# Performance work log

Hardware: AMD Instinct MI355X
Metric: run time of the kernel (lower is better)

## Reference

```python
import jax, jax.numpy as jnp
import numpy as np

CHAN = 128
IN_CHAN = 64
N_LAY = 4
N_OUT = 1000


def _affine_sample(img, theta):
    """F.affine_grid + F.grid_sample (bilinear, zeros padding, align_corners=False).
    img: [B, C, H, W]; theta: [C, 2, 3] (one affine per channel, shared over batch).
    """
    B, C, H, W = img.shape
    dt = img.dtype
    xs = (jnp.arange(W, dtype=dt) + 0.5) * (2.0 / W) - 1.0
    ys = (jnp.arange(H, dtype=dt) + 0.5) * (2.0 / H) - 1.0
    gx, gy = jnp.meshgrid(xs, ys)                      # [H, W] (xy indexing)
    base = jnp.stack([gx, gy, jnp.ones_like(gx)], -1)  # [H, W, 3]
    grid = jnp.einsum('cij,hwj->chwi', theta, base)    # [C, H, W, 2] (x, y)
    ix = ((grid[..., 0] + 1.0) * W - 1.0) * 0.5        # unnormalize, align_corners=False
    iy = ((grid[..., 1] + 1.0) * H - 1.0) * 0.5
    x0 = jnp.floor(ix)
    y0 = jnp.floor(iy)
    wx1 = ix - x0
    wy1 = iy - y0
    x0i = x0.astype(jnp.int32)
    y0i = y0.astype(jnp.int32)
    cidx = jnp.arange(C)[:, None, None]

    def tap(yi, xi, w):
        valid = (xi >= 0) & (xi < W) & (yi >= 0) & (yi < H)
        v = img[:, cidx, jnp.clip(yi, 0, H - 1), jnp.clip(xi, 0, W - 1)]  # [B,C,H,W]
        return v * (w * valid.astype(dt))[None]

    return (tap(y0i, x0i, (1 - wy1) * (1 - wx1))
            + tap(y0i, x0i + 1, (1 - wy1) * wx1)
            + tap(y0i + 1, x0i, wy1 * (1 - wx1))
            + tap(y0i + 1, x0i + 1, wy1 * wx1))


def _geom_layer(x, lin, geo, box):
    # expand-multiply-sum channel mix == einsum
    mixed = jnp.einsum('ci,bihw->bchw', lin, x)        # [B, chan, H, W]
    b = _affine_sample(jnp.ones_like(mixed), box)      # warped box of ones
    w = _affine_sample(mixed, geo)                     # warped features
    return w * b


def setup_inputs() -> dict:
    key = jax.random.key(0)
    ks = jax.random.split(key, 10)
    eye = jnp.eye(3, dtype=jnp.float32)[:2]            # [2, 3]
    x = jax.random.normal(ks[0], (16, IN_CHAN, 96, 96), dtype=jnp.float32)
    in_geo = eye[None] + 0.1 * jax.random.normal(ks[1], (CHAN, 2, 3), dtype=jnp.float32)
    in_box = eye[None] + 0.1 * jax.random.normal(ks[2], (CHAN, 2, 3), dtype=jnp.float32)
    in_lin = jax.random.uniform(ks[3], (CHAN, IN_CHAN), dtype=jnp.float32)
    lay_geo = eye[None, None] + 0.1 * jax.random.normal(ks[4], (N_LAY, CHAN, 2, 3), dtype=jnp.float32)
    lay_box = eye[None, None] + 0.1 * jax.random.normal(ks[5], (N_LAY, CHAN, 2, 3), dtype=jnp.float32)
    lay_lin = jax.random.uniform(ks[6], (N_LAY, CHAN, CHAN), dtype=jnp.float32)
    bound = 1.0 / np.sqrt(CHAN)
    dense_w = jax.random.uniform(ks[7], (N_OUT, CHAN), dtype=jnp.float32, minval=-bound, maxval=bound)
    dense_b = jax.random.uniform(ks[8], (N_OUT,), dtype=jnp.float32, minval=-bound, maxval=bound)
    return {"x": x, "in_geo": in_geo, "in_box": in_box, "in_lin": in_lin,
            "lay_geo": lay_geo, "lay_box": lay_box, "lay_lin": lay_lin,
            "dense_w": dense_w, "dense_b": dense_b}


def reference(x, in_geo, in_box, in_lin, lay_geo, lay_box, lay_lin, dense_w, dense_b):
    x = _geom_layer(x, in_lin, in_geo, in_box)
    for i in range(lay_lin.shape[0]):                  # resCon=True
        x = _geom_layer(x, lay_lin[i], lay_geo[i], lay_box[i]) + x
    feat_maps = x
    pooled = feat_maps.mean(axis=(-2, -1))             # [B, chan]
    logits = pooled @ dense_w.T + dense_b              # [B, nbOut]
    return (logits, feat_maps)
```

## Files before the change

kernel.cpp:

```cpp
#include <hip/hip_runtime.h>
#include <stdint.h>

#define HW 96
#define NPIX 9216
#define NCH 128
#define NB 16
#define HP 98

using bf16x8 = __attribute__((ext_vector_type(8))) short;
using f32x4  = __attribute__((ext_vector_type(4))) float;

__device__ inline uint32_t packbf(float v) {
    uint32_t u  = __float_as_uint(v);
    uint32_t rh = (u + 0x7FFFu + ((u >> 16) & 1u)) & 0xFFFF0000u;
    float    lo = v - __uint_as_float(rh);
    uint32_t ul = __float_as_uint(lo);
    uint32_t rl = ((ul + 0x7FFFu + ((ul >> 16) & 1u)) >> 16) & 0xFFFFu;
    return rh | rl;
}

__global__ __launch_bounds__(256) void packlin_kernel(const float* __restrict__ lin,
                                                      uint32_t* __restrict__ linP, int n) {
    const int i = blockIdx.x * 256 + threadIdx.x;
    if (i < n) linP[i] = packbf(lin[i]);
}

template<int K>
__global__ __launch_bounds__(512, 4) void mix_kernel(const float* __restrict__ x,
                                                     const float* __restrict__ lin,
                                                     float* __restrict__ mixed) {
    const int b    = blockIdx.y;
    const int lane = threadIdx.x & 63;
    const int p    = blockIdx.x * 128 + lane * 2;
    const int c0   = __builtin_amdgcn_readfirstlane((threadIdx.x >> 6) * 16);
    const float* xb = x + (size_t)b * K * NPIX + p;
    const float* lr = lin + c0 * K;

    float2 acc[16];
    #pragma unroll
    for (int c = 0; c < 16; ++c) acc[c] = float2{0.f, 0.f};

    for (int k0 = 0; k0 < K; k0 += 8) {
        float2 xv[8];
        #pragma unroll
        for (int j = 0; j < 8; ++j)
            xv[j] = *(const float2*)&xb[(size_t)(k0 + j) * NPIX];
        #pragma unroll
        for (int c = 0; c < 16; ++c) {
            const float* lc = lr + c * K + k0;
            #pragma unroll
            for (int j = 0; j < 8; ++j) {
                acc[c].x = fmaf(lc[j], xv[j].x, acc[c].x);
                acc[c].y = fmaf(lc[j], xv[j].y, acc[c].y);
            }
        }
    }
    float* ob = mixed + (size_t)b * NCH * NPIX + p;
    #pragma unroll
    for (int c = 0; c < 16; ++c)
        *(float2*)&ob[(size_t)(c0 + c) * NPIX] = acc[c];
}

template<int K>
__global__ __launch_bounds__(512, 2) void mix_mfma_kernel(const float* __restrict__ xf,
                                                          const uint32_t* __restrict__ lp,
                                                          float* __restrict__ mixed) {
    __shared__ uint32_t xs[K * 128];
    const int b   = blockIdx.y;
    const int px0 = blockIdx.x * 128;
    const int t   = threadIdx.x;

    const float* xb = xf + (size_t)b * K * NPIX + px0;
    #pragma unroll
    for (int i = 0; i < K / 16; ++i) {
        const int f4  = i * 512 + t;
        const int row = f4 >> 5;
        const int c4  = (f4 & 31) << 2;
        const float4 v = *(const float4*)&xb[(size_t)row * NPIX + c4];
        uint4 pv;
        pv.x = packbf(v.x); pv.y = packbf(v.y); pv.z = packbf(v.z); pv.w = packbf(v.w);
        *(uint4*)&xs[row * 128 + (c4 ^ ((row & 0xC) << 2))] = pv;
    }

    const int l  = t & 63;
    const int wv = t >> 6;
    const int c0 = wv * 16;
    const int lq = l >> 4;
    const int lr = l & 15;

    constexpr int NQ = K / 32;
    bf16x8 AH[NQ], AL[NQ];
    const uint32_t* lrow = lp + (size_t)(c0 + lr) * K;
    #pragma unroll
    for (int q = 0; q < NQ; ++q) {
        const uint4 a0 = *(const uint4*)&lrow[q * 32 + lq * 4];
        const uint4 a1 = *(const uint4*)&lrow[q * 32 + 16 + lq * 4];
        union { uint32_t w[4]; bf16x8 v; } h, m;
        h.w[0] = (a0.x >> 16) | (a0.y & 0xFFFF0000u);
        h.w[1] = (a0.z >> 16) | (a0.w & 0xFFFF0000u);
        h.w[2] = (a1.x >> 16) | (a1.y & 0xFFFF0000u);
        h.w[3] = (a1.z >> 16) | (a1.w & 0xFFFF0000u);
        m.w[0] = (a0.x & 0xFFFFu) | (a0.y << 16);
        m.w[1] = (a0.z & 0xFFFFu) | (a0.w << 16);
        m.w[2] = (a1.x & 0xFFFFu) | (a1.y << 16);
        m.w[3] = (a1.z & 0xFFFFu) | (a1.w << 16);
        AH[q] = h.v; AL[q] = m.v;
    }

    f32x4 acc[8];
    #pragma unroll
    for (int n = 0; n < 8; ++n) acc[n] = f32x4{0.f, 0.f, 0.f, 0.f};

    __syncthreads();

    const int pswz = lq << 4;
    #pragma unroll
    for (int q = 0; q < NQ; ++q) {
        const int kb = q * 32 + lq * 4;
        #pragma unroll
        for (int np = 0; np < 4; ++np) {
            const int n0 = np * 2;
            bf16x8 BH0, BL0, BH1, BL1;
            #pragma unroll
            for (int s = 0; s < 2; ++s) {
                const int px = ((n0 + s) * 16 + lr) ^ pswz;
                const uint32_t u0 = xs[(kb + 0) * 128 + px];
                const uint32_t u1 = xs[(kb + 1) * 128 + px];
                const uint32_t u2 = xs[(kb + 2) * 128 + px];
                const uint32_t u3 = xs[(kb + 3) * 128 + px];
                const uint32_t u4 = xs[(kb + 16) * 128 + px];
                const uint32_t u5 = xs[(kb + 17) * 128 + px];
                const uint32_t u6 = xs[(kb + 18) * 128 + px];
                const uint32_t u7 = xs[(kb + 19) * 128 + px];
                union { uint32_t w[4]; bf16x8 v; } h, m;
                h.w[0] = (u0 >> 16) | (u1 & 0xFFFF0000u);
                h.w[1] = (u2 >> 16) | (u3 & 0xFFFF0000u);
                h.w[2] = (u4 >> 16) | (u5 & 0xFFFF0000u);
                h.w[3] = (u6 >> 16) | (u7 & 0xFFFF0000u);
                m.w[0] = (u0 & 0xFFFFu) | (u1 << 16);
                m.w[1] = (u2 & 0xFFFFu) | (u3 << 16);
                m.w[2] = (u4 & 0xFFFFu) | (u5 << 16);
                m.w[3] = (u6 & 0xFFFFu) | (u7 << 16);
                if (s == 0) { BH0 = h.v; BL0 = m.v; } else { BH1 = h.v; BL1 = m.v; }
            }
            acc[n0]     = __builtin_amdgcn_mfma_f32_16x16x32_bf16(AH[q], BH0, acc[n0],     0, 0, 0);
            acc[n0 + 1] = __builtin_amdgcn_mfma_f32_16x16x32_bf16(AH[q], BH1, acc[n0 + 1], 0, 0, 0);
            acc[n0]     = __builtin_amdgcn_mfma_f32_16x16x32_bf16(AH[q], BL0, acc[n0],     0, 0, 0);
            acc[n0 + 1] = __builtin_amdgcn_mfma_f32_16x16x32_bf16(AH[q], BL1, acc[n0 + 1], 0, 0, 0);
            acc[n0]     = __builtin_amdgcn_mfma_f32_16x16x32_bf16(AL[q], BH0, acc[n0],     0, 0, 0);
            acc[n0 + 1] = __builtin_amdgcn_mfma_f32_16x16x32_bf16(AL[q], BH1, acc[n0 + 1], 0, 0, 0);
            acc[n0]     = __builtin_amdgcn_mfma_f32_16x16x32_bf16(AL[q], BL0, acc[n0],     0, 0, 0);
            acc[n0 + 1] = __builtin_amdgcn_mfma_f32_16x16x32_bf16(AL[q], BL1, acc[n0 + 1], 0, 0, 0);
        }
    }

    float* ob = mixed + ((size_t)b * NCH + c0 + lq * 4) * NPIX + px0 + lr;
    #pragma unroll
    for (int n = 0; n < 8; ++n)
        #pragma unroll
        for (int r = 0; r < 4; ++r)
            ob[(size_t)r * NPIX + n * 16] = acc[n][r];
}

__device__ inline float clamp01(float z) { return fminf(fmaxf(z, 0.f), 1.f); }

template<bool RES, bool POOL>
__global__ __launch_bounds__(512) void sample_kernel(const float* __restrict__ mixed,
                                                     const float* __restrict__ geo,
                                                     const float* __restrict__ box,
                                                     float* __restrict__ out,
                                                     float* __restrict__ pooled) {
    __shared__ float m[HP * HP];
    const int c = blockIdx.x;
    const int b = blockIdx.y;
    const int t = threadIdx.x;
    if (t < HP) {
        m[t] = 0.f;
        m[(HP - 1) * HP + t] = 0.f;
    } else if (t < HP + 96) {
        const int h = t - HP + 1;
        m[h * HP] = 0.f;
        m[h * HP + HP - 1] = 0.f;
    }
    const float* src = mixed + ((size_t)b * NCH + c) * NPIX;
    #pragma unroll
    for (int r = 0; r < NPIX / 512; ++r) {
        const int idx = r * 512 + t;
        const int h = idx / 96, w = idx - (idx / 96) * 96;
        m[(h + 1) * HP + (w + 1)] = src[idx];
    }
    const float* gth = geo + c * 6;
    const float* bth = box + c * 6;
    const float g0 = gth[0], g1 = gth[1], g3 = gth[3], g4 = gth[4];
    const float gcx = 48.f * gth[2] - 47.5f * (g0 + g1) + 47.5f;
    const float gcy = 48.f * gth[5] - 47.5f * (g3 + g4) + 47.5f;
    const float b0 = bth[0], b1 = bth[1], b3 = bth[3], b4 = bth[4];
    const float bcx = 48.f * bth[2] - 47.5f * (b0 + b1) + 47.5f;
    const float bcy = 48.f * bth[5] - 47.5f * (b3 + b4) + 47.5f;
    float* o = out + ((size_t)b * NCH + c) * NPIX;
    __syncthreads();
    float psum = 0.f;
    #pragma unroll 6
    for (int r = 0; r < NPIX / 512; ++r) {
        const int p = r * 512 + t;
        const int h = p / 96, w = p - (p / 96) * 96;
        const float fw = (float)w, fh = (float)h;
        float ix = fmaf(g0, fw, fmaf(g1, fh, gcx));
        float iy = fmaf(g3, fw, fmaf(g4, fh, gcy));
        ix = fminf(fmaxf(ix, -1.f), 96.f);
        iy = fminf(fmaxf(iy, -1.f), 96.f);
        const float x0f = floorf(ix), y0f = floorf(iy);
        const float fx = ix - x0f, fy = iy - y0f;
        const int base = ((int)y0f + 1) * HP + ((int)x0f + 1);
        const float m00 = m[base],      m01 = m[base + 1];
        const float m10 = m[base + HP], m11 = m[base + HP + 1];
        const float mx0 = fmaf(fx, m01 - m00, m00);
        const float mx1 = fmaf(fx, m11 - m10, m10);
        float v = fmaf(fy, mx1 - mx0, mx0);
        const float bx = fmaf(b0, fw, fmaf(b1, fh, bcx));
        const float by = fmaf(b3, fw, fmaf(b4, fh, bcy));
        const float Xs = fminf(clamp01(bx + 1.f), clamp01(96.f - bx));
        const float Ys = fminf(clamp01(by + 1.f), clamp01(96.f - by));
        v *= Xs * Ys;
        if (RES) v += o[p];
        o[p] = v;
        if (POOL) psum += v;
    }
    if (POOL) {
        #pragma unroll
        for (int off = 32; off > 0; off >>= 1) psum += __shfl_down(psum, off, 64);
        __shared__ float red[8];
        if ((t & 63) == 0) red[t >> 6] = psum;
        __syncthreads();
        if (t == 0) {
            float s = 0.f;
            #pragma unroll
            for (int i = 0; i < 8; ++i) s += red[i];
            pooled[b * NCH + c] = s * (1.f / (float)NPIX);
        }
    }
}

__global__ __launch_bounds__(256) void pool_kernel(const float* __restrict__ feat,
                                                   float* __restrict__ pooled) {
    const int bc = blockIdx.x;
    const float4* f = (const float4*)(feat + (size_t)bc * NPIX);
    float s = 0.f;
    for (int i = threadIdx.x; i < NPIX / 4; i += 256) {
        const float4 v = f[i];
        s += (v.x + v.y) + (v.z + v.w);
    }
    #pragma unroll
    for (int off = 32; off > 0; off >>= 1) s += __shfl_down(s, off, 64);
    __shared__ float red[4];
    if ((threadIdx.x & 63) == 0) red[threadIdx.x >> 6] = s;
    __syncthreads();
    if (threadIdx.x == 0)
        pooled[bc] = (red[0] + red[1] + red[2] + red[3]) * (1.f / (float)NPIX);
}

__global__ __launch_bounds__(256) void dense_kernel(const float* __restrict__ pooled,
                                                    const float* __restrict__ Wt,
                                                    const float* __restrict__ bias,
                                                    float* __restrict__ out) {
    const int idx = blockIdx.x * 256 + threadIdx.x;
    if (idx >= NB * 1000) return;
    const int b = idx / 1000, n = idx - b * 1000;
    float acc = bias[n];
    const float* p = pooled + b * NCH;
    const float* wr = Wt + n * NCH;
    #pragma unroll 4
    for (int c = 0; c < NCH; ++c) acc = fmaf(p[c], wr[c], acc);
    out[idx] = acc;
}

extern "C" void kernel_launch(void* const* d_in, const int* in_sizes, int n_in,
                              void* d_out, int out_size, void* d_ws, size_t ws_size,
                              hipStream_t stream) {
    const float* x       = (const float*)d_in[0];
    const float* in_geo  = (const float*)d_in[1];
    const float* in_box  = (const float*)d_in[2];
    const float* in_lin  = (const float*)d_in[3];
    const float* lay_geo = (const float*)d_in[4];
    const float* lay_box = (const float*)d_in[5];
    const float* lay_lin = (const float*)d_in[6];
    const float* dense_w = (const float*)d_in[7];
    const float* dense_b = (const float*)d_in[8];

    float* out  = (float*)d_out;
    float* feat = out + NB * 1000;
    float* mixed = (float*)d_ws;

    const size_t mixedFloats = (size_t)NB * NCH * NPIX;
    const size_t linPWords   = 4 * NCH * NCH + NCH * 64;
    const bool fusedPool = ws_size >= (mixedFloats + NB * NCH) * sizeof(float);
    const bool mfmaOK    = ws_size >= (mixedFloats + NB * NCH + linPWords) * sizeof(float);
    float* pooled = fusedPool ? (float*)d_ws + mixedFloats : (float*)d_ws;

    const dim3 mixGrid(NPIX / 128, NB);
    const dim3 smpGrid(NCH, NB);

    if (mfmaOK) {
        uint32_t* linP  = (uint32_t*)((float*)d_ws + mixedFloats + NB * NCH);
        uint32_t* linP0 = linP + 4 * NCH * NCH;
        packlin_kernel<<<(4 * NCH * NCH + 255) / 256, 256, 0, stream>>>(lay_lin, linP, 4 * NCH * NCH);
        packlin_kernel<<<(NCH * 64 + 255) / 256, 256, 0, stream>>>(in_lin, linP0, NCH * 64);
        mix_mfma_kernel<64><<<mixGrid, 512, 0, stream>>>(x, linP0, mixed);
        sample_kernel<false, false><<<smpGrid, 512, 0, stream>>>(mixed, in_geo, in_box, feat, pooled);
        for (int i = 0; i < 3; ++i) {
            mix_mfma_kernel<128><<<mixGrid, 512, 0, stream>>>(feat, linP + (size_t)i * NCH * NCH, mixed);
            sample_kernel<true, false><<<smpGrid, 512, 0, stream>>>(mixed, lay_geo + i * NCH * 6,
                                                                    lay_box + i * NCH * 6, feat, pooled);
        }
        mix_mfma_kernel<128><<<mixGrid, 512, 0, stream>>>(feat, linP + (size_t)3 * NCH * NCH, mixed);
        sample_kernel<true, true><<<smpGrid, 512, 0, stream>>>(mixed, lay_geo + 3 * NCH * 6,
                                                               lay_box + 3 * NCH * 6, feat, pooled);
    } else {
        mix_kernel<64><<<mixGrid, 512, 0, stream>>>(x, in_lin, mixed);
        sample_kernel<false, false><<<smpGrid, 512, 0, stream>>>(mixed, in_geo, in_box, feat, pooled);
        for (int i = 0; i < 3; ++i) {
            mix_kernel<128><<<mixGrid, 512, 0, stream>>>(feat, lay_lin + i * NCH * NCH, mixed);
            sample_kernel<true, false><<<smpGrid, 512, 0, stream>>>(mixed, lay_geo + i * NCH * 6,
                                                                    lay_box + i * NCH * 6, feat, pooled);
        }
        mix_kernel<128><<<mixGrid, 512, 0, stream>>>(feat, lay_lin + 3 * NCH * NCH, mixed);
        if (fusedPool) {
            sample_kernel<true, true><<<smpGrid, 512, 0, stream>>>(mixed, lay_geo + 3 * NCH * 6,
                                                                   lay_box + 3 * NCH * 6, feat, pooled);
        } else {
            sample_kernel<true, false><<<smpGrid, 512, 0, stream>>>(mixed, lay_geo + 3 * NCH * 6,
                                                                    lay_box + 3 * NCH * 6, feat, pooled);
            pool_kernel<<<NB * NCH, 256, 0, stream>>>(feat, pooled);
        }
    }
    dense_kernel<<<(NB * 1000 + 255) / 256, 256, 0, stream>>>(pooled, dense_w, dense_b, out);
}
```

Measured before the change: 482.7 us.

## Split MFMA mix into two K-halves overlapping second-half loads with compute

The channel-mix MFMA kernel now loads the input tile in two halves. The second half's global loads are issued before the first half's MFMAs run, and that half is converted and stored to shared memory afterwards, with an extra barrier. The hand-written split-bf16 packing is also replaced by the HIP bf16 conversion intrinsics. The aim is to hide global load latency behind compute and make the conversion cheaper, at the cost of more registers per thread and an additional barrier.

```diff
diff --git a/kernel.cpp b/kernel.cpp
--- a/kernel.cpp
+++ b/kernel.cpp
@@ -1,4 +1,5 @@
 #include <hip/hip_runtime.h>
+#include <hip/hip_bf16.h>
 #include <stdint.h>
 
 #define HW 96
@@ -17,6 +18,15 @@
     uint32_t ul = __float_as_uint(lo);
     uint32_t rl = ((ul + 0x7FFFu + ((ul >> 16) & 1u)) >> 16) & 0xFFFFu;
     return rh | rl;
+}
+
+__device__ inline uint32_t packbf_fast(float v) {
+    __hip_bfloat16 h = __float2bfloat16(v);
+    float hf = __bfloat162float(h);
+    __hip_bfloat16 l = __float2bfloat16(v - hf);
+    union { __hip_bfloat16 b; unsigned short u; } uh, ul;
+    uh.b = h; ul.b = l;
+    return ((uint32_t)uh.u << 16) | (uint32_t)ul.u;
 }
 
 __global__ __launch_bounds__(256) void packlin_kernel(const float* __restrict__ lin,
@@ -70,17 +80,9 @@
     const int px0 = blockIdx.x * 128;
     const int t   = threadIdx.x;
 
+    constexpr int NI = K / 16;
+    constexpr int NQ = K / 32;
     const float* xb = xf + (size_t)b * K * NPIX + px0;
-    #pragma unroll
-    for (int i = 0; i < K / 16; ++i) {
-        const int f4  = i * 512 + t;
-        const int row = f4 >> 5;
-        const int c4  = (f4 & 31) << 2;
-        const float4 v = *(const float4*)&xb[(size_t)row * NPIX + c4];
-        uint4 pv;
-        pv.x = packbf(v.x); pv.y = packbf(v.y); pv.z = packbf(v.z); pv.w = packbf(v.w);
-        *(uint4*)&xs[row * 128 + (c4 ^ ((row & 0xC) << 2))] = pv;
-    }
 
     const int l  = t & 63;
     const int wv = t >> 6;
@@ -88,23 +90,44 @@
     const int lq = l >> 4;
     const int lr = l & 15;
 
-    constexpr int NQ = K / 32;
+    float4 v0[NI / 2];
+    #pragma unroll
+    for (int i = 0; i < NI / 2; ++i) {
+        const int f4  = i * 512 + t;
+        const int row = f4 >> 5;
+        const int c4  = (f4 & 31) << 2;
+        v0[i] = *(const float4*)&xb[(size_t)row * NPIX + c4];
+    }
+
     bf16x8 AH[NQ], AL[NQ];
-    const uint32_t* lrow = lp + (size_t)(c0 + lr) * K;
-    #pragma unroll
-    for (int q = 0; q < NQ; ++q) {
-        const uint4 a0 = *(const uint4*)&lrow[q * 32 + lq * 4];
-        const uint4 a1 = *(const uint4*)&lrow[q * 32 + 16 + lq * 4];
-        union { uint32_t w[4]; bf16x8 v; } h, m;
-        h.w[0] = (a0.x >> 16) | (a0.y & 0xFFFF0000u);
-        h.w[1] = (a0.z >> 16) | (a0.w & 0xFFFF0000u);
-        h.w[2] = (a1.x >> 16) | (a1.y & 0xFFFF0000u);
-        h.w[3] = (a1.z >> 16) | (a1.w & 0xFFFF0000u);
-        m.w[0] = (a0.x & 0xFFFFu) | (a0.y << 16);
-        m.w[1] = (a0.z & 0xFFFFu) | (a0.w << 16);
-        m.w[2] = (a1.x & 0xFFFFu) | (a1.y << 16);
-        m.w[3] = (a1.z & 0xFFFFu) | (a1.w << 16);
-        AH[q] = h.v; AL[q] = m.v;
+    {
+        const uint32_t* lrow = lp + (size_t)(c0 + lr) * K;
+        #pragma unroll
+        for (int q = 0; q < NQ; ++q) {
+            const uint4 a0 = *(const uint4*)&lrow[q * 32 + lq * 4];
+            const uint4 a1 = *(const uint4*)&lrow[q * 32 + 16 + lq * 4];
+            union { uint32_t w[4]; bf16x8 v; } h, m;
+            h.w[0] = (a0.x >> 16) | (a0.y & 0xFFFF0000u);
+            h.w[1] = (a0.z >> 16) | (a0.w & 0xFFFF0000u);
+            h.w[2] = (a1.x >> 16) | (a1.y & 0xFFFF0000u);
+            h.w[3] = (a1.z >> 16) | (a1.w & 0xFFFF0000u);
+            m.w[0] = (a0.x & 0xFFFFu) | (a0.y << 16);
+            m.w[1] = (a0.z & 0xFFFFu) | (a0.w << 16);
+            m.w[2] = (a1.x & 0xFFFFu) | (a1.y << 16);
+            m.w[3] = (a1.z & 0xFFFFu) | (a1.w << 16);
+            AH[q] = h.v; AL[q] = m.v;
+        }
+    }
+
+    #pragma unroll
+    for (int i = 0; i < NI / 2; ++i) {
+        const int f4  = i * 512 + t;
+        const int row = f4 >> 5;
+        const int c4  = (f4 & 31) << 2;
+        uint4 pv;
+        pv.x = packbf_fast(v0[i].x); pv.y = packbf_fast(v0[i].y);
+        pv.z = packbf_fast(v0[i].z); pv.w = packbf_fast(v0[i].w);
+        *(uint4*)&xs[row * 128 + (c4 ^ ((row & 0xC) << 2))] = pv;
     }
 
     f32x4 acc[8];
@@ -114,8 +137,8 @@
     __syncthreads();
 
     const int pswz = lq << 4;
-    #pragma unroll
-    for (int q = 0; q < NQ; ++q) {
+
+    auto compute_q = [&](int q) {
         const int kb = q * 32 + lq * 4;
         #pragma unroll
         for (int np = 0; np < 4; ++np) {
@@ -152,7 +175,34 @@
             acc[n0]     = __builtin_amdgcn_mfma_f32_16x16x32_bf16(AL[q], BL0, acc[n0],     0, 0, 0);
             acc[n0 + 1] = __builtin_amdgcn_mfma_f32_16x16x32_bf16(AL[q], BL1, acc[n0 + 1], 0, 0, 0);
         }
-    }
+    };
+
+    float4 v1[NI / 2];
+    #pragma unroll
+    for (int i = 0; i < NI / 2; ++i) {
+        const int f4  = (NI / 2 + i) * 512 + t;
+        const int row = f4 >> 5;
+        const int c4  = (f4 & 31) << 2;
+        v1[i] = *(const float4*)&xb[(size_t)row * NPIX + c4];
+    }
+
+    #pragma unroll
+    for (int q = 0; q < NQ / 2; ++q) compute_q(q);
+
+    #pragma unroll
+    for (int i = 0; i < NI / 2; ++i) {
+        const int f4  = (NI / 2 + i) * 512 + t;
+        const int row = f4 >> 5;
+        const int c4  = (f4 & 31) << 2;
+        uint4 pv;
+        pv.x = packbf_fast(v1[i].x); pv.y = packbf_fast(v1[i].y);
+        pv.z = packbf_fast(v1[i].z); pv.w = packbf_fast(v1[i].w);
+        *(uint4*)&xs[row * 128 + (c4 ^ ((row & 0xC) << 2))] = pv;
+    }
+    __syncthreads();
+
+    #pragma unroll
+    for (int q = NQ / 2; q < NQ; ++q) compute_q(q);
 
     float* ob = mixed + ((size_t)b * NCH + c0 + lq * 4) * NPIX + px0 + lr;
     #pragma unroll
```

Measured after the change: 439.9 us. 1.1x faster.
